# Kernel optimization log

Hardware: AMD Instinct MI355X
Metric: run time of the kernel (lower is better)

The kernel has to match this reference:

```python
import jax, jax.numpy as jnp
import numpy as np


def setup_inputs() -> dict:
    key = jax.random.key(0)
    ks = jax.random.split(key, 8)
    B, N, D, Dp = 4096, 32, 3, 4
    H, F, Ho = 64, 32, 64
    s = lambda fan: 1.0 / np.sqrt(fan)
    return {
        "xs": jax.random.normal(ks[0], (B, N, D), jnp.float32),
        "xs_pair": jax.random.normal(ks[1], (B, N, N, Dp), jnp.float32),
        "W1p": jax.random.normal(ks[2], (2 * D + Dp, H), jnp.float32) * s(2 * D + Dp),
        "b1p": jnp.zeros((H,), jnp.float32),
        "W2p": jax.random.normal(ks[3], (H, F), jnp.float32) * s(H),
        "b2p": jnp.zeros((F,), jnp.float32),
        "W1o": jax.random.normal(ks[4], (F, Ho), jnp.float32) * s(F),
        "b1o": jnp.zeros((Ho,), jnp.float32),
        "W2o": jax.random.normal(ks[5], (Ho, 1), jnp.float32) * s(Ho),
        "b2o": jnp.zeros((1,), jnp.float32),
    }


def reference(xs, xs_pair, W1p, b1p, W2p, b2p, W1o, b1o, W2o, b2o):
    N = xs.shape[-2]
    i, j = np.triu_indices(N, k=1)  # static pair index lists, P = N(N-1)/2

    def pair_net(x1, x2, x12):
        # small MLP on concatenated pair features: [B, P, 2D+Dp] -> [B, P, F]
        h = jnp.tanh(jnp.concatenate([x1, x2, x12], axis=-1) @ W1p + b1p)
        return h @ W2p + b2p

    xi = xs[:, i]            # [B, P, D]
    xj = xs[:, j]            # [B, P, D]
    xij = xs_pair[:, i, j]   # [B, P, Dp]

    # antisymmetric pairwise net, then product-reduce over pairs -> [B, F]
    zs = jnp.prod(pair_net(xi, xj, xij) - pair_net(xj, xi, xij), axis=-2)

    def odd_net(z):
        return jnp.tanh(z @ W1o + b1o) @ W2o + b2o

    return odd_net(zs) - odd_net(-zs)  # [B, 1]
```

## Files before the change

### kernel.cpp

```cpp
#include <hip/hip_runtime.h>
#include <math.h>


#define NB 4096
#define NN 32

typedef float f32x4 __attribute__((ext_vector_type(4)));
typedef short bf16x8 __attribute__((ext_vector_type(8)));

__device__ __forceinline__ unsigned fbits(float x) { union { float f; unsigned u; } c; c.f = x; return c.u; }
__device__ __forceinline__ float bfloat(unsigned u) { union { float f; unsigned u; } c; c.u = u; return c.f; }

__global__ __launch_bounds__(256, 4) void laughlin_kernel(
    const float* __restrict__ xs,
    const float* __restrict__ xs_pair,
    const float* __restrict__ W1p,
    const float* __restrict__ b1p,
    const float* __restrict__ W2p,
    const float* __restrict__ W1o,
    const float* __restrict__ b1o,
    const float* __restrict__ W2o,
    float* __restrict__ out)
{
    __shared__ f32x4          ldsX[4][NN];
    __shared__ unsigned short ldsHi[4][16][72];
    __shared__ unsigned short ldsLo[4][16][72];
    __shared__ double         ldsZ[4][32];

    const int tid  = threadIdx.x;
    const int wv   = tid >> 6;
    const int lane = tid & 63;
    const int b    = blockIdx.x * 4 + wv;

    const float S = 2.8853900817779268f;
    const float wa0 = S * W1p[0 * 64 + lane], wa1 = S * W1p[1 * 64 + lane], wa2 = S * W1p[2 * 64 + lane];
    const float wb0 = S * W1p[3 * 64 + lane], wb1 = S * W1p[4 * 64 + lane], wb2 = S * W1p[5 * 64 + lane];
    const float wc0 = S * W1p[6 * 64 + lane], wc1 = S * W1p[7 * 64 + lane], wc2 = S * W1p[8 * 64 + lane];
    const float wc3 = S * W1p[9 * 64 + lane];
    const float b1S = S * b1p[lane];

    const int m  = lane & 15;
    const int g  = lane >> 4;
    bf16x8 bhi[2][2], blo[2][2];
    #pragma unroll
    for (int t = 0; t < 2; ++t)
      #pragma unroll
      for (int s = 0; s < 2; ++s) {
        bf16x8 h, l;
        #pragma unroll
        for (int e = 0; e < 8; ++e) {
          const float w = 2.0f * W2p[(32 * s + g * 8 + e) * 32 + (m + 16 * t)];
          const unsigned u = fbits(w);
          h[e] = (short)(u >> 16);
          const float lof = w - bfloat(u & 0xFFFF0000u);
          l[e] = (short)(fbits(lof) >> 16);
        }
        bhi[t][s] = h; blo[t][s] = l;
      }

    if (lane < NN) {
        const float* p = xs + ((size_t)b * NN + lane) * 3;
        f32x4 v; v.x = p[0]; v.y = p[1]; v.z = p[2]; v.w = 0.f;
        ldsX[wv][lane] = v;
    }
    __builtin_amdgcn_wave_barrier();

    const f32x4* xp4 = (const f32x4*)(xs_pair + (size_t)b * (NN * NN * 4));
    double pp0 = 1.0, pp1 = 1.0;
    int i = 0, j = 1, ip = -1;
    float aI = 0.f, bI = 0.f;

    for (int bt = 0; bt < 31; ++bt) {
        #pragma unroll 4
        for (int q = 0; q < 16; ++q) {
            if (i != ip) {
                const f32x4 xi = ldsX[wv][i];
                aI = fmaf(xi.z, wa2, fmaf(xi.y, wa1, xi.x * wa0));
                bI = fmaf(xi.z, wb2, fmaf(xi.y, wb1, xi.x * wb0));
                ip = i;
            }
            const f32x4 xj = ldsX[wv][j];
            const float aJ = fmaf(xj.z, wa2, fmaf(xj.y, wa1, xj.x * wa0));
            const float bJ = fmaf(xj.z, wb2, fmaf(xj.y, wb1, xj.x * wb0));
            const f32x4 xij = xp4[(i << 5) + j];
            const float c = fmaf(xij.w, wc3, fmaf(xij.z, wc2,
                            fmaf(xij.y, wc1, fmaf(xij.x, wc0, b1S))));
            const float p1 = (aI + c) + bJ;
            const float p2 = (aJ + c) + bI;
            const float e1 = __builtin_amdgcn_exp2f(p1);
            const float e2 = __builtin_amdgcn_exp2f(p2);
            const float d  = (e1 - e2) * __builtin_amdgcn_rcpf((e1 + 1.f) * (e2 + 1.f));
            const unsigned u = fbits(d);
            ldsHi[wv][q][lane] = (unsigned short)(u >> 16);
            const float lof = d - bfloat(u & 0xFFFF0000u);
            ldsLo[wv][q][lane] = (unsigned short)(fbits(lof) >> 16);
            if (++j == NN) { ++i; j = i + 1; }
        }
        __builtin_amdgcn_wave_barrier();

        const bf16x8 ah0 = *(const bf16x8*)&ldsHi[wv][m][g * 8];
        const bf16x8 ah1 = *(const bf16x8*)&ldsHi[wv][m][32 + g * 8];
        const bf16x8 al0 = *(const bf16x8*)&ldsLo[wv][m][g * 8];
        const bf16x8 al1 = *(const bf16x8*)&ldsLo[wv][m][32 + g * 8];
        __builtin_amdgcn_wave_barrier();

        f32x4 acc0 = {0.f, 0.f, 0.f, 0.f};
        f32x4 acc1 = {0.f, 0.f, 0.f, 0.f};
        acc0 = __builtin_amdgcn_mfma_f32_16x16x32_bf16(al0, bhi[0][0], acc0, 0, 0, 0);
        acc0 = __builtin_amdgcn_mfma_f32_16x16x32_bf16(ah0, blo[0][0], acc0, 0, 0, 0);
        acc0 = __builtin_amdgcn_mfma_f32_16x16x32_bf16(ah0, bhi[0][0], acc0, 0, 0, 0);
        acc0 = __builtin_amdgcn_mfma_f32_16x16x32_bf16(al1, bhi[0][1], acc0, 0, 0, 0);
        acc0 = __builtin_amdgcn_mfma_f32_16x16x32_bf16(ah1, blo[0][1], acc0, 0, 0, 0);
        acc0 = __builtin_amdgcn_mfma_f32_16x16x32_bf16(ah1, bhi[0][1], acc0, 0, 0, 0);
        acc1 = __builtin_amdgcn_mfma_f32_16x16x32_bf16(al0, bhi[1][0], acc1, 0, 0, 0);
        acc1 = __builtin_amdgcn_mfma_f32_16x16x32_bf16(ah0, blo[1][0], acc1, 0, 0, 0);
        acc1 = __builtin_amdgcn_mfma_f32_16x16x32_bf16(ah0, bhi[1][0], acc1, 0, 0, 0);
        acc1 = __builtin_amdgcn_mfma_f32_16x16x32_bf16(al1, bhi[1][1], acc1, 0, 0, 0);
        acc1 = __builtin_amdgcn_mfma_f32_16x16x32_bf16(ah1, blo[1][1], acc1, 0, 0, 0);
        acc1 = __builtin_amdgcn_mfma_f32_16x16x32_bf16(ah1, bhi[1][1], acc1, 0, 0, 0);

        const float q0 = (acc0[0] * acc0[1]) * (acc0[2] * acc0[3]);
        const float q1 = (acc1[0] * acc1[1]) * (acc1[2] * acc1[3]);
        pp0 *= (double)q0;
        pp1 *= (double)q1;
    }

    pp0 *= __shfl_xor(pp0, 16);  pp0 *= __shfl_xor(pp0, 32);
    pp1 *= __shfl_xor(pp1, 16);  pp1 *= __shfl_xor(pp1, 32);
    if (lane < 16) { ldsZ[wv][lane] = pp0; ldsZ[wv][lane + 16] = pp1; }
    __builtin_amdgcn_wave_barrier();

    double hacc = 0.0;
    #pragma unroll
    for (int f = 0; f < 32; ++f) hacc = fma(ldsZ[wv][f], (double)W1o[f * 64 + lane], hacc);
    const double bo = (double)b1o[lane];
    const double u2 = tanh(hacc + bo) - tanh(bo - hacc);
    double y = u2 * (double)W2o[lane];
    #pragma unroll
    for (int off = 32; off; off >>= 1) y += __shfl_xor(y, off);
    if (lane == 0) out[b] = (float)y;
}

extern "C" void kernel_launch(void* const* d_in, const int* in_sizes, int n_in,
                              void* d_out, int out_size, void* d_ws, size_t ws_size,
                              hipStream_t stream) {
    const float* xs      = (const float*)d_in[0];
    const float* xs_pair = (const float*)d_in[1];
    const float* W1p     = (const float*)d_in[2];
    const float* b1p     = (const float*)d_in[3];
    const float* W2p     = (const float*)d_in[4];
    const float* W1o     = (const float*)d_in[6];
    const float* b1o     = (const float*)d_in[7];
    const float* W2o     = (const float*)d_in[8];
    float* out = (float*)d_out;

    hipLaunchKernelGGL(laughlin_kernel, dim3(NB / 4), dim3(256), 0, stream,
                       xs, xs_pair, W1p, b1p, W2p, W1o, b1o, W2o, out);
}
```

Before: 305.1 us.

## Split each batch row's pairs across two waves with prefetched pair loads

Each batch row is now handled by two waves that split the 496 pairs by parity, and their partial products are combined through shared memory. A pair-index table built in LDS lets each wave do one coalesced prefetch of the next 16 xs_pair vectors and broadcast them with shuffles, replacing a dependent global load per pair. The grid doubles, the occupancy hint rises to 5, and a fourth lo*lo MFMA term is added for precision. In exchange the kernel needs block-wide syncs, extra shuffles, and more MFMA work per tile.

```diff
diff --git a/kernel.cpp b/kernel.cpp
--- a/kernel.cpp
+++ b/kernel.cpp
@@ -11,7 +11,7 @@
 __device__ __forceinline__ unsigned fbits(float x) { union { float f; unsigned u; } c; c.f = x; return c.u; }
 __device__ __forceinline__ float bfloat(unsigned u) { union { float f; unsigned u; } c; c.u = u; return c.f; }
 
-__global__ __launch_bounds__(256, 4) void laughlin_kernel(
+__global__ __launch_bounds__(256, 5) void laughlin_kernel(
     const float* __restrict__ xs,
     const float* __restrict__ xs_pair,
     const float* __restrict__ W1p,
@@ -22,15 +22,20 @@
     const float* __restrict__ W2o,
     float* __restrict__ out)
 {
-    __shared__ f32x4          ldsX[4][NN];
+    __shared__ f32x4          ldsX[2][NN];
     __shared__ unsigned short ldsHi[4][16][72];
     __shared__ unsigned short ldsLo[4][16][72];
-    __shared__ double         ldsZ[4][32];
+    __shared__ unsigned short ldsTbl[2][256];
+    __shared__ double         ldsPP[2][2][32];
 
     const int tid  = threadIdx.x;
     const int wv   = tid >> 6;
     const int lane = tid & 63;
-    const int b    = blockIdx.x * 4 + wv;
+    const int row  = __builtin_amdgcn_readfirstlane(wv >> 1);
+    const int h    = __builtin_amdgcn_readfirstlane(wv & 1);
+    const int b    = blockIdx.x * 2 + row;
+    const int m    = lane & 15;
+    const int g    = lane >> 4;
 
     const float S = 2.8853900817779268f;
     const float wa0 = S * W1p[0 * 64 + lane], wa1 = S * W1p[1 * 64 + lane], wa2 = S * W1p[2 * 64 + lane];
@@ -39,65 +44,76 @@
     const float wc3 = S * W1p[9 * 64 + lane];
     const float b1S = S * b1p[lane];
 
-    const int m  = lane & 15;
-    const int g  = lane >> 4;
     bf16x8 bhi[2][2], blo[2][2];
     #pragma unroll
     for (int t = 0; t < 2; ++t)
       #pragma unroll
       for (int s = 0; s < 2; ++s) {
-        bf16x8 h, l;
+        bf16x8 hh, ll;
         #pragma unroll
         for (int e = 0; e < 8; ++e) {
           const float w = 2.0f * W2p[(32 * s + g * 8 + e) * 32 + (m + 16 * t)];
           const unsigned u = fbits(w);
-          h[e] = (short)(u >> 16);
-          const float lof = w - bfloat(u & 0xFFFF0000u);
-          l[e] = (short)(fbits(lof) >> 16);
+          hh[e] = (short)(u >> 16);
+          ll[e] = (short)(fbits(w - bfloat(u & 0xFFFF0000u)) >> 16);
         }
-        bhi[t][s] = h; blo[t][s] = l;
+        bhi[t][s] = hh; blo[t][s] = ll;
       }
 
-    if (lane < NN) {
-        const float* p = xs + ((size_t)b * NN + lane) * 3;
-        f32x4 v; v.x = p[0]; v.y = p[1]; v.z = p[2]; v.w = 0.f;
-        ldsX[wv][lane] = v;
+    if (wv < 2) {
+        if (lane < NN) {
+            const float* p = xs + ((size_t)(blockIdx.x * 2 + wv) * NN + lane) * 3;
+            f32x4 v; v.x = p[0]; v.y = p[1]; v.z = p[2]; v.w = 0.f;
+            ldsX[wv][lane] = v;
+        }
+    } else {
+        const int hh = wv - 2;
+        for (int n = lane; n < 256; n += 64) {
+            int p = 2 * n + hh; if (p > 494 + hh) p = 494 + hh;
+            const double sd = sqrt((double)(3969 - 8 * p));
+            const int i  = (int)((63.0 - sd) * 0.5);
+            const int fi = 31 * i - ((i * (i - 1)) >> 1);
+            const int j  = p - fi + i + 1;
+            ldsTbl[hh][n] = (unsigned short)((i << 5) | j);
+        }
     }
-    __builtin_amdgcn_wave_barrier();
+    __syncthreads();
 
     const f32x4* xp4 = (const f32x4*)(xs_pair + (size_t)b * (NN * NN * 4));
+    f32x4 cur = xp4[ldsTbl[h][m]];
+    f32x4 nxt;
+
     double pp0 = 1.0, pp1 = 1.0;
-    int i = 0, j = 1, ip = -1;
-    float aI = 0.f, bI = 0.f;
+    int i = 0, j = 1 + h, ip = -1;
+    float aI = 0.f, bIv = 0.f;
 
-    for (int bt = 0; bt < 31; ++bt) {
-        #pragma unroll 4
-        for (int q = 0; q < 16; ++q) {
-            if (i != ip) {
-                const f32x4 xi = ldsX[wv][i];
-                aI = fmaf(xi.z, wa2, fmaf(xi.y, wa1, xi.x * wa0));
-                bI = fmaf(xi.z, wb2, fmaf(xi.y, wb1, xi.x * wb0));
-                ip = i;
-            }
-            const f32x4 xj = ldsX[wv][j];
-            const float aJ = fmaf(xj.z, wa2, fmaf(xj.y, wa1, xj.x * wa0));
-            const float bJ = fmaf(xj.z, wb2, fmaf(xj.y, wb1, xj.x * wb0));
-            const f32x4 xij = xp4[(i << 5) + j];
-            const float c = fmaf(xij.w, wc3, fmaf(xij.z, wc2,
-                            fmaf(xij.y, wc1, fmaf(xij.x, wc0, b1S))));
-            const float p1 = (aI + c) + bJ;
-            const float p2 = (aJ + c) + bI;
-            const float e1 = __builtin_amdgcn_exp2f(p1);
-            const float e2 = __builtin_amdgcn_exp2f(p2);
-            const float d  = (e1 - e2) * __builtin_amdgcn_rcpf((e1 + 1.f) * (e2 + 1.f));
-            const unsigned u = fbits(d);
-            ldsHi[wv][q][lane] = (unsigned short)(u >> 16);
-            const float lof = d - bfloat(u & 0xFFFF0000u);
-            ldsLo[wv][q][lane] = (unsigned short)(fbits(lof) >> 16);
-            if (++j == NN) { ++i; j = i + 1; }
+    auto do_pair = [&](int q) {
+        if (i != ip) {
+            const f32x4 xi = ldsX[row][i];
+            aI  = fmaf(xi.z, wa2, fmaf(xi.y, wa1, xi.x * wa0));
+            bIv = fmaf(xi.z, wb2, fmaf(xi.y, wb1, xi.x * wb0));
+            ip = i;
         }
+        const f32x4 xj = ldsX[row][j];
+        const float aJ = fmaf(xj.z, wa2, fmaf(xj.y, wa1, xj.x * wa0));
+        const float bJ = fmaf(xj.z, wb2, fmaf(xj.y, wb1, xj.x * wb0));
+        const float cx = __shfl(cur.x, q), cy = __shfl(cur.y, q);
+        const float cz = __shfl(cur.z, q), cw = __shfl(cur.w, q);
+        const float c = fmaf(cw, wc3, fmaf(cz, wc2, fmaf(cy, wc1, fmaf(cx, wc0, b1S))));
+        const float p1 = (aI + c) + bJ;
+        const float p2 = (aJ + c) + bIv;
+        const float e1 = __builtin_amdgcn_exp2f(p1);
+        const float e2 = __builtin_amdgcn_exp2f(p2);
+        const float d  = (e1 - e2) * __builtin_amdgcn_rcpf((e1 + 1.f) * (e2 + 1.f));
+        const unsigned u = fbits(d);
+        ldsHi[wv][q][lane] = (unsigned short)(u >> 16);
+        ldsLo[wv][q][lane] = (unsigned short)(fbits(d - bfloat(u & 0xFFFF0000u)) >> 16);
+        j += 2;
+        if (j >= NN) { ++i; j = i + 1 + (j - NN); }
+    };
+
+    auto do_mfma = [&](bool tail) {
         __builtin_amdgcn_wave_barrier();
-
         const bf16x8 ah0 = *(const bf16x8*)&ldsHi[wv][m][g * 8];
         const bf16x8 ah1 = *(const bf16x8*)&ldsHi[wv][m][32 + g * 8];
         const bf16x8 al0 = *(const bf16x8*)&ldsLo[wv][m][g * 8];
@@ -106,39 +122,61 @@
 
         f32x4 acc0 = {0.f, 0.f, 0.f, 0.f};
         f32x4 acc1 = {0.f, 0.f, 0.f, 0.f};
+        acc0 = __builtin_amdgcn_mfma_f32_16x16x32_bf16(al0, blo[0][0], acc0, 0, 0, 0);
         acc0 = __builtin_amdgcn_mfma_f32_16x16x32_bf16(al0, bhi[0][0], acc0, 0, 0, 0);
         acc0 = __builtin_amdgcn_mfma_f32_16x16x32_bf16(ah0, blo[0][0], acc0, 0, 0, 0);
         acc0 = __builtin_amdgcn_mfma_f32_16x16x32_bf16(ah0, bhi[0][0], acc0, 0, 0, 0);
+        acc0 = __builtin_amdgcn_mfma_f32_16x16x32_bf16(al1, blo[0][1], acc0, 0, 0, 0);
         acc0 = __builtin_amdgcn_mfma_f32_16x16x32_bf16(al1, bhi[0][1], acc0, 0, 0, 0);
         acc0 = __builtin_amdgcn_mfma_f32_16x16x32_bf16(ah1, blo[0][1], acc0, 0, 0, 0);
         acc0 = __builtin_amdgcn_mfma_f32_16x16x32_bf16(ah1, bhi[0][1], acc0, 0, 0, 0);
+        acc1 = __builtin_amdgcn_mfma_f32_16x16x32_bf16(al0, blo[1][0], acc1, 0, 0, 0);
         acc1 = __builtin_amdgcn_mfma_f32_16x16x32_bf16(al0, bhi[1][0], acc1, 0, 0, 0);
         acc1 = __builtin_amdgcn_mfma_f32_16x16x32_bf16(ah0, blo[1][0], acc1, 0, 0, 0);
         acc1 = __builtin_amdgcn_mfma_f32_16x16x32_bf16(ah0, bhi[1][0], acc1, 0, 0, 0);
+        acc1 = __builtin_amdgcn_mfma_f32_16x16x32_bf16(al1, blo[1][1], acc1, 0, 0, 0);
         acc1 = __builtin_amdgcn_mfma_f32_16x16x32_bf16(al1, bhi[1][1], acc1, 0, 0, 0);
         acc1 = __builtin_amdgcn_mfma_f32_16x16x32_bf16(ah1, blo[1][1], acc1, 0, 0, 0);
         acc1 = __builtin_amdgcn_mfma_f32_16x16x32_bf16(ah1, bhi[1][1], acc1, 0, 0, 0);
 
-        const float q0 = (acc0[0] * acc0[1]) * (acc0[2] * acc0[3]);
-        const float q1 = (acc1[0] * acc1[1]) * (acc1[2] * acc1[3]);
+        float q0 = (acc0[0] * acc0[1]) * (acc0[2] * acc0[3]);
+        float q1 = (acc1[0] * acc1[1]) * (acc1[2] * acc1[3]);
+        if (tail && g >= 2) { q0 = 1.0f; q1 = 1.0f; }
         pp0 *= (double)q0;
         pp1 *= (double)q1;
+    };
+
+    for (int bt = 0; bt < 15; ++bt) {
+        int n2 = 16 * (bt + 1) + m; if (n2 > 247) n2 = 247;
+        nxt = xp4[ldsTbl[h][n2]];
+        #pragma unroll
+        for (int q = 0; q < 16; ++q) do_pair(q);
+        do_mfma(false);
+        cur = nxt;
     }
+    #pragma unroll
+    for (int q = 0; q < 8; ++q) do_pair(q);
+    do_mfma(true);
 
     pp0 *= __shfl_xor(pp0, 16);  pp0 *= __shfl_xor(pp0, 32);
     pp1 *= __shfl_xor(pp1, 16);  pp1 *= __shfl_xor(pp1, 32);
-    if (lane < 16) { ldsZ[wv][lane] = pp0; ldsZ[wv][lane + 16] = pp1; }
-    __builtin_amdgcn_wave_barrier();
+    if (lane < 16) { ldsPP[row][h][lane] = pp0; ldsPP[row][h][lane + 16] = pp1; }
+    __syncthreads();
 
-    double hacc = 0.0;
-    #pragma unroll
-    for (int f = 0; f < 32; ++f) hacc = fma(ldsZ[wv][f], (double)W1o[f * 64 + lane], hacc);
-    const double bo = (double)b1o[lane];
-    const double u2 = tanh(hacc + bo) - tanh(bo - hacc);
-    double y = u2 * (double)W2o[lane];
-    #pragma unroll
-    for (int off = 32; off; off >>= 1) y += __shfl_xor(y, off);
-    if (lane == 0) out[b] = (float)y;
+    if (h == 0) {
+        double hacc = 0.0;
+        #pragma unroll
+        for (int f = 0; f < 32; ++f) {
+            const double zf = ldsPP[row][0][f] * ldsPP[row][1][f];
+            hacc = fma(zf, (double)W1o[f * 64 + lane], hacc);
+        }
+        const double bo = (double)b1o[lane];
+        const double u2 = tanh(hacc + bo) - tanh(bo - hacc);
+        double y = u2 * (double)W2o[lane];
+        #pragma unroll
+        for (int off = 32; off; off >>= 1) y += __shfl_xor(y, off);
+        if (lane == 0) out[b] = (float)y;
+    }
 }
 
 extern "C" void kernel_launch(void* const* d_in, const int* in_sizes, int n_in,
@@ -154,6 +192,6 @@
     const float* W2o     = (const float*)d_in[8];
     float* out = (float*)d_out;
 
-    hipLaunchKernelGGL(laughlin_kernel, dim3(NB / 4), dim3(256), 0, stream,
+    hipLaunchKernelGGL(laughlin_kernel, dim3(NB / 2), dim3(256), 0, stream,
                        xs, xs_pair, W1p, b1p, W2p, W1o, b1o, W2o, out);
 }
```

Measured after the change: 250.6 us. -17.9%, faster.
